# Optimization experiments

Hardware: AMD Instinct MI355X
Metric: run time of the kernel (lower is better)

Reference implementation:

```python
import jax, jax.numpy as jnp
import numpy as np

NNODES = 8192
DIM = 64
K = 32
ALPHA = 3.0


def setup_inputs() -> dict:
    key = jax.random.key(0)
    ks = jax.random.split(key, 7)
    idx = jnp.arange(NNODES, dtype=jnp.int64)
    # xavier_uniform for 2D params, uniform[0,1) for biases (per _reset_parameters)
    def xavier(k, shape):
        fan_in, fan_out = shape[1], shape[0]
        bound = float(np.sqrt(6.0 / (fan_in + fan_out)))
        return jax.random.uniform(k, shape, jnp.float32, -bound, bound)
    E1 = xavier(ks[0], (NNODES, DIM))
    E2 = xavier(ks[1], (NNODES, DIM))
    W1 = xavier(ks[2], (DIM, DIM))
    b1 = jax.random.uniform(ks[3], (DIM,), jnp.float32)
    W2 = xavier(ks[4], (DIM, DIM))
    b2 = jax.random.uniform(ks[5], (DIM,), jnp.float32)
    return {"idx": idx, "E1": E1, "E2": E2, "W1": W1, "b1": b1, "W2": W2, "b2": b2}


def reference(idx, E1, E2, W1, b1, W2, b2):
    n = idx.shape[0]
    # embedding lookups [n, dim]
    v1 = E1[idx]
    v2 = E2[idx]
    # linear (torch: x @ W.T + b) then tanh saturation
    v1 = jnp.tanh(ALPHA * (v1 @ W1.T + b1))
    v2 = jnp.tanh(ALPHA * (v2 @ W2.T + b2))
    # antisymmetric score matrix [n, n]
    a = v1 @ v2.T - v2 @ v1.T
    A = jax.nn.relu(jnp.tanh(ALPHA * a))
    # top-k per row -> binary mask via scatter
    _, t1 = jax.lax.top_k(A, K)  # [n, K]
    rows = jnp.arange(n)[:, None]
    mask = jnp.zeros((n, n), A.dtype).at[rows, t1].set(1.0)
    return A * mask
```

## Files before the change

### kernel.cpp

```cpp
#include <hip/hip_runtime.h>
#include <stdint.h>
#include <math.h>

#define NN 8192
#define DIM 64
#define KSEL 32
#define BK2 8
#define TILE 128
#define NTB (NN / TILE)
#define NTRI ((NTB * (NTB + 1)) / 2)

#define AS1 __attribute__((address_space(1)))
#define AS3 __attribute__((address_space(3)))
typedef float v2f __attribute__((ext_vector_type(2)));

__device__ __forceinline__ v2f pk_fma(v2f a, v2f b, v2f c) {
#if __has_builtin(__builtin_elementwise_fma)
    return __builtin_elementwise_fma(a, b, c);
#else
    v2f r; r.x = fmaf(a.x, b.x, c.x); r.y = fmaf(a.y, b.y, c.y); return r;
#endif
}

__device__ __forceinline__ float tanh_xla(float x) {
    const float kClamp = 7.90531110763549805f;
    float xc = fminf(fmaxf(x, -kClamp), kClamp);
    float x2 = xc * xc;
    float p = -2.76076847742355e-16f;
    p = fmaf(x2, p, 2.00018790482477e-13f);
    p = fmaf(x2, p, -8.60467152213735e-11f);
    p = fmaf(x2, p, 5.12229709037114e-08f);
    p = fmaf(x2, p, 1.48572235717979e-05f);
    p = fmaf(x2, p, 6.37261928875436e-04f);
    p = fmaf(x2, p, 4.89352455891786e-03f);
    p = xc * p;
    float q = 1.19825839466702e-06f;
    q = fmaf(x2, q, 1.18534705686654e-04f);
    q = fmaf(x2, q, 2.26843463243900e-03f);
    q = fmaf(x2, q, 4.89352518554385e-03f);
    float r = p / q;
    return (fabsf(x) < 0.0004f) ? x : r;
}
__device__ __forceinline__ float tanh_xla_pos(float ax) {
    const float kClamp = 7.90531110763549805f;
    float xc = fminf(ax, kClamp);
    float x2 = xc * xc;
    float p = -2.76076847742355e-16f;
    p = fmaf(x2, p, 2.00018790482477e-13f);
    p = fmaf(x2, p, -8.60467152213735e-11f);
    p = fmaf(x2, p, 5.12229709037114e-08f);
    p = fmaf(x2, p, 1.48572235717979e-05f);
    p = fmaf(x2, p, 6.37261928875436e-04f);
    p = fmaf(x2, p, 4.89352455891786e-03f);
    p = xc * p;
    float q = 1.19825839466702e-06f;
    q = fmaf(x2, q, 1.18534705686654e-04f);
    q = fmaf(x2, q, 2.26843463243900e-03f);
    q = fmaf(x2, q, 4.89352518554385e-03f);
    float r = p / q;
    return (ax < 0.0004f) ? ax : r;
}

__global__ __launch_bounds__(256) void k_embed(
    const int* __restrict__ gidx,
    const float* __restrict__ E1, const float* __restrict__ E2,
    const float* __restrict__ W1, const float* __restrict__ b1,
    const float* __restrict__ W2, const float* __restrict__ b2,
    float* __restrict__ VT1, float* __restrict__ VT2)
{
    __shared__ float W1s[DIM][DIM + 1];
    __shared__ float W2s[DIM][DIM + 1];
    __shared__ float E1s[4][DIM];
    __shared__ float E2s[4][DIM];
    __shared__ float T1[DIM][5];
    __shared__ float T2[DIM][5];
    const int t = threadIdx.x;
    for (int i = t; i < DIM * DIM; i += 256) {
        W1s[i >> 6][i & 63] = W1[i];
        W2s[i >> 6][i & 63] = W2[i];
    }
    const int rbase = blockIdx.x * 4;
    for (int i = t; i < 4 * DIM; i += 256) {
        const int r = i >> 6, k = i & 63;
        const int g = gidx[rbase + r];
        E1s[r][k] = E1[(size_t)g * DIM + k];
        E2s[r][k] = E2[(size_t)g * DIM + k];
    }
    __syncthreads();
    const int o = t & 63, rs = t >> 6;
    float m1 = 0.0f, m2 = 0.0f;
    #pragma unroll
    for (int k = 0; k < DIM; ++k) {
        m1 = fmaf(E1s[rs][k], W1s[o][k], m1);
        m2 = fmaf(E2s[rs][k], W2s[o][k], m2);
    }
    T1[o][rs] = tanh_xla(3.0f * (m1 + b1[o]));
    T2[o][rs] = tanh_xla(3.0f * (m2 + b2[o]));
    __syncthreads();
    const int oo = t >> 2, rr = t & 3;
    VT1[(size_t)oo * NN + rbase + rr] = T1[oo][rr];
    VT2[(size_t)oo * NN + rbase + rr] = T2[oo][rr];
}

__global__ __launch_bounds__(256, 3) void k_score(
    const float* __restrict__ VT1, const float* __restrict__ VT2,
    float* __restrict__ out)
{
    const int L = blockIdx.x;
    int bi = (int)(64.5f - sqrtf(fmaf(-2.0f, (float)L, 64.5f * 64.5f)));
    while (bi * NTB - (bi * (bi - 1)) / 2 > L) --bi;
    while ((bi + 1) * NTB - ((bi + 1) * bi) / 2 <= L) ++bi;
    const int bj = bi + (L - (bi * NTB - (bi * (bi - 1)) / 2));

    __shared__ __align__(16) float lds[2][4][BK2][TILE];

    const int t = threadIdx.x;
    const int tx = t & 15;
    const int ty = t >> 4;
    const int Ibase = bi * TILE, Jbase = bj * TILE;

    const int w = t >> 6, l = t & 63;
    const float* vt = (w & 1) ? VT2 : VT1;
    const int cbase = (w & 2) ? Jbase : Ibase;
    const int srow = (l >> 5);
    const int scol = (l & 31) * 4;

    v2f acc1[8][4], acc2[8][4];
    #pragma unroll
    for (int i = 0; i < 8; ++i)
        #pragma unroll
        for (int j = 0; j < 4; ++j) { acc1[i][j] = (v2f)(0.0f); acc2[i][j] = (v2f)(0.0f); }

    #pragma unroll
    for (int p = 0; p < 4; ++p) {
        const float* src = vt + (size_t)(2 * p + srow) * NN + cbase + scol;
        __builtin_amdgcn_global_load_lds((AS1 const void*)src,
                                         (AS3 void*)&lds[0][w][2 * p + srow][scol], 16, 0, 0);
    }
    __syncthreads();

    for (int c8 = 0; c8 < 8; ++c8) {
        const int cur = c8 & 1;
        if (c8 < 7) {
            const int ckn = (c8 + 1) * BK2;
            #pragma unroll
            for (int p = 0; p < 4; ++p) {
                const float* src = vt + (size_t)(ckn + 2 * p + srow) * NN + cbase + scol;
                __builtin_amdgcn_global_load_lds((AS1 const void*)src,
                                                 (AS3 void*)&lds[cur ^ 1][w][2 * p + srow][scol], 16, 0, 0);
            }
        }
        #pragma unroll 2
        for (int k = 0; k < BK2; ++k) {
            const float4 fa1l = *(const float4*)&lds[cur][0][k][ty * 8];
            const float4 fa1h = *(const float4*)&lds[cur][0][k][ty * 8 + 4];
            const float4 fa2l = *(const float4*)&lds[cur][1][k][ty * 8];
            const float4 fa2h = *(const float4*)&lds[cur][1][k][ty * 8 + 4];
            const float4 fb1l = *(const float4*)&lds[cur][2][k][tx * 4];
            const float4 fb1h = *(const float4*)&lds[cur][2][k][tx * 4 + 64];
            const float4 fb2l = *(const float4*)&lds[cur][3][k][tx * 4];
            const float4 fb2h = *(const float4*)&lds[cur][3][k][tx * 4 + 64];
            v2f c1p[4], c2p[4];
            c1p[0] = (v2f){fb1l.x, fb1l.y}; c1p[1] = (v2f){fb1l.z, fb1l.w};
            c1p[2] = (v2f){fb1h.x, fb1h.y}; c1p[3] = (v2f){fb1h.z, fb1h.w};
            c2p[0] = (v2f){fb2l.x, fb2l.y}; c2p[1] = (v2f){fb2l.z, fb2l.w};
            c2p[2] = (v2f){fb2h.x, fb2h.y}; c2p[3] = (v2f){fb2h.z, fb2h.w};
            float a1[8] = {fa1l.x, fa1l.y, fa1l.z, fa1l.w, fa1h.x, fa1h.y, fa1h.z, fa1h.w};
            float a2[8] = {fa2l.x, fa2l.y, fa2l.z, fa2l.w, fa2h.x, fa2h.y, fa2h.z, fa2h.w};
            #pragma unroll
            for (int i = 0; i < 8; ++i) {
                const v2f a1v = (v2f){a1[i], a1[i]};
                const v2f a2v = (v2f){a2[i], a2[i]};
                #pragma unroll
                for (int jp = 0; jp < 4; ++jp) {
                    acc1[i][jp] = pk_fma(a1v, c2p[jp], acc1[i][jp]);
                    acc2[i][jp] = pk_fma(a2v, c1p[jp], acc2[i][jp]);
                }
            }
        }
        __syncthreads();
    }

    #pragma unroll
    for (int i = 0; i < 8; ++i)
        #pragma unroll
        for (int jp = 0; jp < 4; ++jp)
            #pragma unroll
            for (int e = 0; e < 2; ++e) {
                const float aa = acc1[i][jp][e] - acc2[i][jp][e];
                const float tt = tanh_xla_pos(3.0f * fabsf(aa));
                acc1[i][jp][e] = (aa > 0.0f) ? tt : 0.0f;
                acc2[i][jp][e] = (aa < 0.0f) ? tt : 0.0f;
            }
    #pragma unroll
    for (int i = 0; i < 8; ++i) {
        const int gi = Ibase + ty * 8 + i;
        *(float4*)&out[(size_t)gi * NN + Jbase + tx * 4] =
            make_float4(acc1[i][0][0], acc1[i][0][1], acc1[i][1][0], acc1[i][1][1]);
        *(float4*)&out[(size_t)gi * NN + Jbase + 64 + tx * 4] =
            make_float4(acc1[i][2][0], acc1[i][2][1], acc1[i][3][0], acc1[i][3][1]);
    }
    if (bi != bj) {
        #pragma unroll
        for (int jp = 0; jp < 4; ++jp)
            #pragma unroll
            for (int e = 0; e < 2; ++e) {
                const int j = jp * 2 + e;
                const int gj = Jbase + tx * 4 + (j >> 2) * 64 + (j & 3);
                float4* p = (float4*)&out[(size_t)gj * NN + Ibase + ty * 8];
                p[0] = make_float4(acc2[0][jp][e], acc2[1][jp][e], acc2[2][jp][e], acc2[3][jp][e]);
                p[1] = make_float4(acc2[4][jp][e], acc2[5][jp][e], acc2[6][jp][e], acc2[7][jp][e]);
            }
    }
}

__global__ __launch_bounds__(256) void k_topk(float* __restrict__ out)
{
    __shared__ uint32_t hist[4][2048];
    __shared__ uint32_t waveTot[4];
    __shared__ uint32_t bc_bin, bc_ca, bc_m, bc_flag;

    const int row = blockIdx.x;
    const int t = threadIdx.x;
    const int wid = t >> 6, lane = t & 63;
    float* rp = out + (size_t)row * NN;

    float v[32];
    #pragma unroll
    for (int s = 0; s < 8; ++s) {
        const float4 f = *(const float4*)&rp[(s * 256 + t) * 4];
        v[s*4+0] = f.x; v[s*4+1] = f.y; v[s*4+2] = f.z; v[s*4+3] = f.w;
    }
    if (t == 0) bc_flag = 0;

    uint64_t prefix = 0, thr = 0;
    int need = KSEL;
    bool done = false;

    for (int pass = 0; pass < 4; ++pass) {
        const int shift = 33 - 11 * pass;
        {
            const uint4 z = make_uint4(0u, 0u, 0u, 0u);
            uint4* hp = (uint4*)hist;
            #pragma unroll
            for (int i = 0; i < 8; ++i) hp[i * 256 + t] = z;
        }
        __syncthreads();
        #pragma unroll
        for (int s = 0; s < 8; ++s) {
            #pragma unroll
            for (int e = 0; e < 4; ++e) {
                const uint32_t vb = __float_as_uint(v[s*4+e]);
                if (vb == 0u) continue;
                const int gi = s * 1024 + t * 4 + e;
                const uint64_t key = ((uint64_t)vb << 13) | (uint32_t)(8191 - gi);
                if ((key >> (shift + 11)) == prefix)
                    atomicAdd(&hist[wid][(uint32_t)((key >> shift) & 2047u)], 1u);
            }
        }
        __syncthreads();
        uint32_t m[8]; uint32_t tot = 0;
        #pragma unroll
        for (int i = 0; i < 8; ++i) {
            const int b = t * 8 + i;
            m[i] = hist[0][b] + hist[1][b] + hist[2][b] + hist[3][b];
            tot += m[i];
        }
        uint32_t ssum = tot;
        #pragma unroll
        for (int d = 1; d < 64; d <<= 1) {
            const uint32_t o = __shfl_down(ssum, d, 64);
            if (lane + d < 64) ssum += o;
        }
        if (lane == 0) waveTot[wid] = ssum;
        __syncthreads();
        {
            uint32_t above = 0;
            for (int w2 = wid + 1; w2 < 4; ++w2) above += waveTot[w2];
            if (pass == 0) {
                const uint32_t totalAll = waveTot[0] + waveTot[1] + waveTot[2] + waveTot[3];
                if (totalAll < (uint32_t)need && t == 0) bc_flag = 1;
            }
            uint32_t c = (ssum - tot) + above;
            #pragma unroll
            for (int i = 7; i >= 0; --i) {
                if (c < (uint32_t)need && (uint32_t)need <= c + m[i]) {
                    bc_bin = (uint32_t)(t * 8 + i);
                    bc_ca  = c;
                    bc_m   = m[i];
                }
                c += m[i];
            }
        }
        __syncthreads();
        if (bc_flag) { thr = 1; done = true; }
        else {
            prefix = (prefix << 11) | (uint64_t)bc_bin;
            need  -= (int)bc_ca;
            if ((uint32_t)need == bc_m) {
                thr = prefix << shift;
                done = true;
            } else if (pass == 3) { thr = prefix; done = true; }
        }
        if (done) break;
        __syncthreads();
    }

    #pragma unroll
    for (int s = 0; s < 8; ++s) {
        float w[4];
        #pragma unroll
        for (int e = 0; e < 4; ++e) {
            const float a = v[s*4+e];
            const uint32_t vb = __float_as_uint(a);
            const int gi = s * 1024 + t * 4 + e;
            const uint64_t key = ((uint64_t)vb << 13) | (uint32_t)(8191 - gi);
            w[e] = (vb != 0u && key >= thr) ? a : 0.f;
        }
        *(float4*)&rp[(s * 256 + t) * 4] = make_float4(w[0], w[1], w[2], w[3]);
    }
}

extern "C" void kernel_launch(void* const* d_in, const int* in_sizes, int n_in,
                              void* d_out, int out_size, void* d_ws, size_t ws_size,
                              hipStream_t stream)
{
    const int*   idx = (const int*)  d_in[0];
    const float* E1  = (const float*)d_in[1];
    const float* E2  = (const float*)d_in[2];
    const float* W1  = (const float*)d_in[3];
    const float* b1  = (const float*)d_in[4];
    const float* W2  = (const float*)d_in[5];
    const float* b2  = (const float*)d_in[6];
    float* out = (float*)d_out;
    float* VT1 = (float*)d_ws;
    float* VT2 = VT1 + (size_t)NN * DIM;

    k_embed<<<NN / 4, 256, 0, stream>>>(idx, E1, E2, W1, b1, W2, b2, VT1, VT2);
    k_score<<<NTRI, 256, 0, stream>>>(VT1, VT2, out);
    k_topk<<<NN, 256, 0, stream>>>(out);
}
```

Baseline: 295.7 us.

## Double score k-chunk depth and add saturated-row fast path to top-k

The score kernel's k-chunk doubles from 8 to 16, halving the number of pipeline stages and barriers, and the min-occupancy launch bound is dropped. The top-k kernel gains a fast path: when a row's max equals the saturated tanh constant and at least K entries hit it, a binary search over index finds the first K saturated entries and writes the result directly. This skips the multi-pass radix histogram. The fast path is only taken when the saturated case actually occurs, and the larger LDS buffer may reduce occupancy.

```diff
diff --git a/kernel.cpp b/kernel.cpp
--- a/kernel.cpp
+++ b/kernel.cpp
@@ -5,7 +5,7 @@
 #define NN 8192
 #define DIM 64
 #define KSEL 32
-#define BK2 8
+#define BK2 16
 #define TILE 128
 #define NTB (NN / TILE)
 #define NTRI ((NTB * (NTB + 1)) / 2)
@@ -102,7 +102,7 @@
     VT2[(size_t)oo * NN + rbase + rr] = T2[oo][rr];
 }
 
-__global__ __launch_bounds__(256, 3) void k_score(
+__global__ __launch_bounds__(256) void k_score(
     const float* __restrict__ VT1, const float* __restrict__ VT2,
     float* __restrict__ out)
 {
@@ -132,19 +132,19 @@
         for (int j = 0; j < 4; ++j) { acc1[i][j] = (v2f)(0.0f); acc2[i][j] = (v2f)(0.0f); }
 
     #pragma unroll
-    for (int p = 0; p < 4; ++p) {
+    for (int p = 0; p < 8; ++p) {
         const float* src = vt + (size_t)(2 * p + srow) * NN + cbase + scol;
         __builtin_amdgcn_global_load_lds((AS1 const void*)src,
                                          (AS3 void*)&lds[0][w][2 * p + srow][scol], 16, 0, 0);
     }
     __syncthreads();
 
-    for (int c8 = 0; c8 < 8; ++c8) {
-        const int cur = c8 & 1;
-        if (c8 < 7) {
-            const int ckn = (c8 + 1) * BK2;
-            #pragma unroll
-            for (int p = 0; p < 4; ++p) {
+    for (int c4 = 0; c4 < 4; ++c4) {
+        const int cur = c4 & 1;
+        if (c4 < 3) {
+            const int ckn = (c4 + 1) * BK2;
+            #pragma unroll
+            for (int p = 0; p < 8; ++p) {
                 const float* src = vt + (size_t)(ckn + 2 * p + srow) * NN + cbase + scol;
                 __builtin_amdgcn_global_load_lds((AS1 const void*)src,
                                                  (AS3 void*)&lds[cur ^ 1][w][2 * p + srow][scol], 16, 0, 0);
@@ -218,6 +218,7 @@
 {
     __shared__ uint32_t hist[4][2048];
     __shared__ uint32_t waveTot[4];
+    __shared__ uint32_t redc[4], redm[4];
     __shared__ uint32_t bc_bin, bc_ca, bc_m, bc_flag;
 
     const int row = blockIdx.x;
@@ -232,6 +233,71 @@
         v[s*4+0] = f.x; v[s*4+1] = f.y; v[s*4+2] = f.z; v[s*4+3] = f.w;
     }
     if (t == 0) bc_flag = 0;
+
+    const uint32_t Cb = __float_as_uint(tanh_xla_pos(8.0f));
+
+    uint32_t isC = 0, maxv = 0;
+    #pragma unroll
+    for (int s = 0; s < 8; ++s)
+        #pragma unroll
+        for (int e = 0; e < 4; ++e) {
+            const uint32_t vb = __float_as_uint(v[s*4+e]);
+            if (vb == Cb) isC |= (1u << (s * 4 + e));
+            maxv = vb > maxv ? vb : maxv;
+        }
+    {
+        uint32_t c = (uint32_t)__popc(isC), m = maxv;
+        #pragma unroll
+        for (int d = 1; d < 64; d <<= 1) {
+            c += (uint32_t)__shfl_down((int)c, d, 64);
+            const uint32_t om = (uint32_t)__shfl_down((int)m, d, 64);
+            m = om > m ? om : m;
+        }
+        if (lane == 0) { redc[wid] = c; redm[wid] = m; }
+    }
+    __syncthreads();
+    const uint32_t cntC = redc[0] + redc[1] + redc[2] + redc[3];
+    uint32_t mAll = redm[0];
+    mAll = redm[1] > mAll ? redm[1] : mAll;
+    mAll = redm[2] > mAll ? redm[2] : mAll;
+    mAll = redm[3] > mAll ? redm[3] : mAll;
+    __syncthreads();
+
+    if (mAll == Cb && cntC >= (uint32_t)KSEL) {
+        int lo = 0, hi = NN;
+        while (hi - lo > 1) {
+            const int mid = (lo + hi) >> 1;
+            uint32_t mask = 0;
+            #pragma unroll
+            for (int s = 0; s < 8; ++s) {
+                const int base = s * 1024 + t * 4;
+                int d = mid - base;
+                d = d < 0 ? 0 : (d > 4 ? 4 : d);
+                mask |= ((1u << d) - 1u) << (s * 4);
+            }
+            int c = __popc(isC & mask);
+            #pragma unroll
+            for (int d = 1; d < 64; d <<= 1) c += __shfl_down(c, d, 64);
+            if (lane == 0) redc[wid] = (uint32_t)c;
+            __syncthreads();
+            const int tot = (int)(redc[0] + redc[1] + redc[2] + redc[3]);
+            if (tot >= KSEL) hi = mid; else lo = mid;
+            __syncthreads();
+        }
+        const int xstar = hi;
+        #pragma unroll
+        for (int s = 0; s < 8; ++s) {
+            float w[4];
+            #pragma unroll
+            for (int e = 0; e < 4; ++e) {
+                const float a = v[s*4+e];
+                const int gi = s * 1024 + t * 4 + e;
+                w[e] = (__float_as_uint(a) == Cb && gi < xstar) ? a : 0.f;
+            }
+            *(float4*)&rp[(s * 256 + t) * 4] = make_float4(w[0], w[1], w[2], w[3]);
+        }
+        return;
+    }
 
     uint64_t prefix = 0, thr = 0;
     int need = KSEL;
```

Measured after the change: 289.9 us. About the same (-1.9%).
